# Performance work log

Measured on AMD Instinct MI355X. Metric: run time of the kernel, lower is better.

Reference implementation:

```python
import jax, jax.numpy as jnp
import numpy as np

B, T, F = 256, 288, 64
UNITS = [128, 64, 64, 32]
SCALE = 0.05  # small init so relu-activated recurrence stays numerically stable


def _lstm_scan(x_tbf, Wk, Wr, b):
    """Keras LSTM with activation=relu, recurrent_activation=sigmoid.
    x_tbf: [T, B, in]. Returns all hidden states [T, B, u].
    Gate order in the fused kernel is (i, f, g, o), as in Keras."""
    u = Wr.shape[0]
    bsz = x_tbf.shape[1]

    def step(carry, xt):
        h, c = carry
        z = xt @ Wk + h @ Wr + b            # [B, 4u]
        i, f, g, o = jnp.split(z, 4, axis=-1)
        i = jax.nn.sigmoid(i)
        f = jax.nn.sigmoid(f)
        g = jax.nn.relu(g)                   # cell-input activation = relu
        o = jax.nn.sigmoid(o)
        c = f * c + i * g
        h = o * jax.nn.relu(c)               # output activation = relu
        return (h, c), h

    init = (jnp.zeros((bsz, u), x_tbf.dtype), jnp.zeros((bsz, u), x_tbf.dtype))
    _, hs = jax.lax.scan(step, init, x_tbf)
    return hs  # [T, B, u]


def setup_inputs() -> dict:
    key = jax.random.key(0)
    ks = jax.random.split(key, 20)
    out = {"x": jax.random.normal(ks[0], (B, T, F), dtype=jnp.float32)}
    ins = [F] + UNITS[:-1]
    ki = 1
    for li, (din, u) in enumerate(zip(ins, UNITS), start=1):
        out[f"W{li}"] = jax.random.normal(ks[ki], (din, 4 * u), jnp.float32) * SCALE; ki += 1
        out[f"U{li}"] = jax.random.normal(ks[ki], (u, 4 * u), jnp.float32) * SCALE; ki += 1
        out[f"b{li}"] = jnp.zeros((4 * u,), jnp.float32)
    out["Wf"] = jax.random.normal(ks[ki], (UNITS[-1], 16), jnp.float32) * SCALE; ki += 1
    out["bf"] = jnp.zeros((16,), jnp.float32)
    out["Wo"] = jax.random.normal(ks[ki], (16, 1), jnp.float32) * SCALE
    out["bo"] = jnp.zeros((1,), jnp.float32)
    return out


def reference(x, W1, U1, b1, W2, U2, b2, W3, U3, b3, W4, U4, b4, Wf, bf, Wo, bo):
    # Dropout layers are identity at inference (Keras deterministic call).
    h = jnp.transpose(x, (1, 0, 2))          # [T, B, F] time-major for scan
    h = _lstm_scan(h, W1, U1, b1)            # [T, B, 128]
    h = _lstm_scan(h, W2, U2, b2)            # [T, B, 64]
    h = _lstm_scan(h, W3, U3, b3)            # [T, B, 64]
    h_last = _lstm_scan(h, W4, U4, b4)[-1]   # [B, 32] (return_sequences=False)
    fc = jax.nn.relu(h_last @ Wf + bf)       # [B, 16]
    return fc @ Wo + bo                      # [B, 1]
```

## Files before the change

kernel.cpp:

```cpp
#include <hip/hip_runtime.h>
#include <math.h>

#define TSTEPS 288
#define NTHREADS 512

typedef float f32x2 __attribute__((ext_vector_type(2)));

__device__ __forceinline__ float sigmoidf_(float x) {
    return 1.0f / (1.0f + __expf(-x));
}

__device__ __forceinline__ void pkfma(f32x2& acc, f32x2 w, f32x2 x) {
    asm("v_pk_fma_f32 %0, %1, %2, %0" : "+v"(acc) : "v"(w), "v"(x));
}

template<int NS>
__device__ __forceinline__ float allreduce_seg(float v) {
    if constexpr (NS > 1)
        v += __int_as_float(__builtin_amdgcn_update_dpp(
                0, __float_as_int(v), 0xB1, 0xF, 0xF, true));
    if constexpr (NS > 2)
        v += __int_as_float(__builtin_amdgcn_update_dpp(
                0, __float_as_int(v), 0x4E, 0xF, 0xF, true));
    if constexpr (NS > 4)
        v += __int_as_float(__builtin_amdgcn_ds_swizzle(
                __float_as_int(v), 0x101F));
    return v;
}

template<int NS, int KSEG>
__device__ __forceinline__ int perm_idx(int j) {
    return (((j % KSEG) >> 2) * NS + (j / KSEG)) * 4 + (j & 3);
}

template<int DIN, int U, int NS, int ACTIVE, int SEQNS, int SEQK,
         bool FIRST, bool WRITE_NOW, bool WRITE_DELAY>
__device__ void run_layer(const float* __restrict__ Wk,
                          const float* __restrict__ Wr,
                          const float* __restrict__ bias,
                          const float* __restrict__ xg,
                          float* __restrict__ seq,
                          float* __restrict__ xh,
                          float* __restrict__ xring,
                          int tid)
{
    constexpr int KIN  = DIN / NS;
    constexpr int KH   = U / NS;
    constexpr int COLS = 4 * U;
    constexpr int S    = (NS == 4) ? 2 : 3;
    constexpr int NPI  = KIN / 2;
    constexpr int NPH  = KH / 2;
    static_assert(ACTIVE == NS * U, "thread mapping");
    static_assert(KIN % 4 == 0 && (KH % 4 == 0), "float4 alignment");
    static_assert(NS <= 8, "butterfly width");

    const int seg = tid & (NS - 1);
    const int u   = tid >> S;
    const bool act = tid < ACTIVE;

    f32x2 w[4][NPI + NPH];
    float bz[4] = {0.f, 0.f, 0.f, 0.f};
    float cst = 0.0f, hprev = 0.0f;

    if (act) {
#pragma unroll
        for (int p = 0; p < NPI; ++p) {
            const int k0 = seg * KIN + 2 * p;
#pragma unroll
            for (int g = 0; g < 4; ++g) {
                const int c = g * U + u;
                w[g][p] = f32x2{Wk[(size_t)k0 * COLS + c],
                                Wk[(size_t)(k0 + 1) * COLS + c]};
            }
        }
#pragma unroll
        for (int p = 0; p < NPH; ++p) {
            const int k0 = seg * KH + 2 * p;
#pragma unroll
            for (int g = 0; g < 4; ++g) {
                const int c = g * U + u;
                w[g][NPI + p] = f32x2{Wr[(size_t)k0 * COLS + c],
                                      Wr[(size_t)(k0 + 1) * COLS + c]};
            }
        }
        if (seg == 0) {
#pragma unroll
            for (int g = 0; g < 4; ++g) bz[g] = bias[g * U + u];
        }
#pragma unroll
        for (int g = 0; g < 4; ++g)
#pragma unroll
            for (int p = 0; p < NPI + NPH; ++p)
                asm volatile("" : "+v"(w[g][p]));
    }
    if (tid < 128) xh[tid] = 0.0f;
    if (FIRST && tid < 64)
        xring[perm_idx<4, 16>(tid)] = xg[tid];
    __syncthreads();

    for (int t = 0; t < TSTEPS; ++t) {
        if (act) {
            const float* __restrict__ xr = xh + (t & 1) * 128;
            float* __restrict__ xw       = xh + ((t + 1) & 1) * 128;

            float xstage = 0.0f;
            if (FIRST && tid < 64 && (t + 1) < TSTEPS)
                xstage = xg[(t + 1) * 64 + tid];

            f32x2 ac0 = {0.f, 0.f}, ac1 = {0.f, 0.f},
                  ac2 = {0.f, 0.f}, ac3 = {0.f, 0.f};

            {
                const float4* in4 = reinterpret_cast<const float4*>(
                    FIRST ? (xring + (t & 1) * 64) : (seq + t * 128)) + seg;
#pragma unroll
                for (int k4 = 0; k4 < KIN / 4; ++k4) {
                    const float4 v = in4[k4 * NS];
                    const f32x2 lo = {v.x, v.y}, hi = {v.z, v.w};
                    pkfma(ac0, w[0][2*k4+0], lo); pkfma(ac0, w[0][2*k4+1], hi);
                    pkfma(ac1, w[1][2*k4+0], lo); pkfma(ac1, w[1][2*k4+1], hi);
                    pkfma(ac2, w[2][2*k4+0], lo); pkfma(ac2, w[2][2*k4+1], hi);
                    pkfma(ac3, w[3][2*k4+0], lo); pkfma(ac3, w[3][2*k4+1], hi);
                }
            }
            {
                const float4* h4 = reinterpret_cast<const float4*>(xr) + seg;
#pragma unroll
                for (int k4 = 0; k4 < KH / 4; ++k4) {
                    const float4 v = h4[k4 * NS];
                    const f32x2 lo = {v.x, v.y}, hi = {v.z, v.w};
                    const int pb = NPI + 2 * k4;
                    pkfma(ac0, w[0][pb], lo); pkfma(ac0, w[0][pb+1], hi);
                    pkfma(ac1, w[1][pb], lo); pkfma(ac1, w[1][pb+1], hi);
                    pkfma(ac2, w[2][pb], lo); pkfma(ac2, w[2][pb+1], hi);
                    pkfma(ac3, w[3][pb], lo); pkfma(ac3, w[3][pb+1], hi);
                }
            }

            float a0 = (ac0[0] + ac0[1]) + bz[0];
            float a1 = (ac1[0] + ac1[1]) + bz[1];
            float a2 = (ac2[0] + ac2[1]) + bz[2];
            float a3 = (ac3[0] + ac3[1]) + bz[3];
            a0 = allreduce_seg<NS>(a0);
            a1 = allreduce_seg<NS>(a1);
            a2 = allreduce_seg<NS>(a2);
            a3 = allreduce_seg<NS>(a3);

            if constexpr (WRITE_DELAY) {
                if (seg == 0 && t > 0)
                    seq[(t - 1) * 128 + perm_idx<SEQNS, SEQK>(u)] = hprev;
            }

            const float gi = sigmoidf_(a0);
            const float gf = sigmoidf_(a1);
            const float gg = fmaxf(a2, 0.0f);
            const float go = sigmoidf_(a3);
            cst = fmaf(gf, cst, gi * gg);
            const float h = go * fmaxf(cst, 0.0f);

            if (seg == 0) {
                xw[perm_idx<NS, KH>(u)] = h;
                if constexpr (WRITE_NOW)
                    seq[t * 128 + perm_idx<SEQNS, SEQK>(u)] = h;
            }
            hprev = h;

            if (FIRST && tid < 64 && (t + 1) < TSTEPS)
                xring[((t + 1) & 1) * 64 + perm_idx<4, 16>(tid)] = xstage;
        }
        __syncthreads();
    }

    if constexpr (WRITE_DELAY) {
        if (act && seg == 0)
            seq[(TSTEPS - 1) * 128 + perm_idx<SEQNS, SEQK>(u)] = hprev;
    }
}

extern "C" __global__ void __launch_bounds__(NTHREADS, 2)
lstm_stack_kernel(const float* __restrict__ x,
                  const float* __restrict__ W1, const float* __restrict__ U1, const float* __restrict__ b1,
                  const float* __restrict__ W2, const float* __restrict__ U2, const float* __restrict__ b2,
                  const float* __restrict__ W3, const float* __restrict__ U3, const float* __restrict__ b3,
                  const float* __restrict__ W4, const float* __restrict__ U4, const float* __restrict__ b4,
                  const float* __restrict__ Wf, const float* __restrict__ bf,
                  const float* __restrict__ Wo, const float* __restrict__ bo,
                  float* __restrict__ out)
{
    __shared__ __align__(16) float seq[TSTEPS * 128];
    __shared__ __align__(16) float xh[256 + 16];
    __shared__ __align__(16) float xring[2 * 64];

    const int tid = threadIdx.x;
    const float* xg = x + (size_t)blockIdx.x * TSTEPS * 64;

    run_layer< 64, 128, 4, 512,  8, 16, true , true , false>(W1, U1, b1, xg, seq, xh, xring, tid);
    __syncthreads();
    run_layer<128,  64, 8, 512,  8,  8, false, false, true >(W2, U2, b2, xg, seq, xh, xring, tid);
    __syncthreads();
    run_layer< 64,  64, 8, 512,  8,  8, false, false, true >(W3, U3, b3, xg, seq, xh, xring, tid);
    __syncthreads();
    run_layer< 64,  32, 8, 256,  8,  8, false, false, false>(W4, U4, b4, xg, seq, xh, xring, tid);
    __syncthreads();

    if (tid < 16) {
        float acc = bf[tid];
#pragma unroll
        for (int k = 0; k < 32; ++k) acc = fmaf(xh[k], Wf[k * 16 + tid], acc);
        xh[256 + tid] = fmaxf(acc, 0.0f);
    }
    __syncthreads();
    if (tid == 0) {
        float acc = bo[0];
#pragma unroll
        for (int k = 0; k < 16; ++k) acc = fmaf(xh[256 + k], Wo[k], acc);
        out[blockIdx.x] = acc;
    }
}

extern "C" void kernel_launch(void* const* d_in, const int* in_sizes, int n_in,
                              void* d_out, int out_size, void* d_ws, size_t ws_size,
                              hipStream_t stream) {
    const float* x  = (const float*)d_in[0];
    const float* W1 = (const float*)d_in[1];
    const float* U1 = (const float*)d_in[2];
    const float* b1 = (const float*)d_in[3];
    const float* W2 = (const float*)d_in[4];
    const float* U2 = (const float*)d_in[5];
    const float* b2 = (const float*)d_in[6];
    const float* W3 = (const float*)d_in[7];
    const float* U3 = (const float*)d_in[8];
    const float* b3 = (const float*)d_in[9];
    const float* W4 = (const float*)d_in[10];
    const float* U4 = (const float*)d_in[11];
    const float* b4 = (const float*)d_in[12];
    const float* Wf = (const float*)d_in[13];
    const float* bf = (const float*)d_in[14];
    const float* Wo = (const float*)d_in[15];
    const float* bo = (const float*)d_in[16];
    float* out = (float*)d_out;

    lstm_stack_kernel<<<dim3(256), dim3(NTHREADS), 0, stream>>>(
        x, W1, U1, b1, W2, U2, b2, W3, U3, b3, W4, U4, b4, Wf, bf, Wo, bo, out);
}
```

Measured before the change: 713.5 us.

## Split gate columns across thread pairs and double block size to 1024

Each hidden unit's four gate columns are now split across two thread groups (i,f vs g,o), halving per-thread weights and FMAs and doubling the block to 1024 threads. After the segmented reduction, the pair exchanges gate pre-activations with a ds_swizzle so both halves can compute the cell update, and only one writes h. This shortens the serial per-step critical path of the recurrence, at the cost of an extra cross-lane exchange, a wider __syncthreads barrier each timestep, and launch bounds of 4 waves per SIMD that constrain register use.

```diff
diff --git a/kernel.cpp b/kernel.cpp
--- a/kernel.cpp
+++ b/kernel.cpp
@@ -2,7 +2,7 @@
 #include <math.h>
 
 #define TSTEPS 288
-#define NTHREADS 512
+#define NTHREADS 1024
 
 typedef float f32x2 __attribute__((ext_vector_type(2)));
 
@@ -26,6 +26,12 @@
         v += __int_as_float(__builtin_amdgcn_ds_swizzle(
                 __float_as_int(v), 0x101F));
     return v;
+}
+
+template<int NS>
+__device__ __forceinline__ float swz_pair(float v) {
+    return __int_as_float(__builtin_amdgcn_ds_swizzle(
+        __float_as_int(v), (NS << 10) | 0x1F));
 }
 
 template<int NS, int KSEG>
@@ -47,51 +53,49 @@
     constexpr int KIN  = DIN / NS;
     constexpr int KH   = U / NS;
     constexpr int COLS = 4 * U;
-    constexpr int S    = (NS == 4) ? 2 : 3;
+    constexpr int LOG  = (NS == 4) ? 2 : 3;
     constexpr int NPI  = KIN / 2;
     constexpr int NPH  = KH / 2;
-    static_assert(ACTIVE == NS * U, "thread mapping");
-    static_assert(KIN % 4 == 0 && (KH % 4 == 0), "float4 alignment");
-    static_assert(NS <= 8, "butterfly width");
+    constexpr int NP   = NPI + NPH;
+    static_assert(ACTIVE == 2 * U * NS, "thread mapping");
+    static_assert(KIN % 4 == 0 && KH % 4 == 0, "float4 alignment");
+    static_assert(NS == 4 || NS == 8, "butterfly width");
 
     const int seg = tid & (NS - 1);
-    const int u   = tid >> S;
+    const int p   = (tid >> LOG) & 1;
+    const int u   = tid >> (LOG + 1);
     const bool act = tid < ACTIVE;
 
-    f32x2 w[4][NPI + NPH];
-    float bz[4] = {0.f, 0.f, 0.f, 0.f};
+    f32x2 w[2][NP];
+    float bz[2] = {0.f, 0.f};
     float cst = 0.0f, hprev = 0.0f;
 
     if (act) {
-#pragma unroll
-        for (int p = 0; p < NPI; ++p) {
-            const int k0 = seg * KIN + 2 * p;
-#pragma unroll
-            for (int g = 0; g < 4; ++g) {
-                const int c = g * U + u;
-                w[g][p] = f32x2{Wk[(size_t)k0 * COLS + c],
-                                Wk[(size_t)(k0 + 1) * COLS + c]};
-            }
+        const int colA = (2 * p) * U + u;
+        const int colB = (2 * p + 1) * U + u;
+#pragma unroll
+        for (int q = 0; q < NPI; ++q) {
+            const int k0 = seg * KIN + 2 * q;
+            w[0][q] = f32x2{Wk[(size_t)k0 * COLS + colA],
+                            Wk[(size_t)(k0 + 1) * COLS + colA]};
+            w[1][q] = f32x2{Wk[(size_t)k0 * COLS + colB],
+                            Wk[(size_t)(k0 + 1) * COLS + colB]};
         }
 #pragma unroll
-        for (int p = 0; p < NPH; ++p) {
-            const int k0 = seg * KH + 2 * p;
-#pragma unroll
-            for (int g = 0; g < 4; ++g) {
-                const int c = g * U + u;
-                w[g][NPI + p] = f32x2{Wr[(size_t)k0 * COLS + c],
-                                      Wr[(size_t)(k0 + 1) * COLS + c]};
-            }
+        for (int q = 0; q < NPH; ++q) {
+            const int k0 = seg * KH + 2 * q;
+            w[0][NPI + q] = f32x2{Wr[(size_t)k0 * COLS + colA],
+                                  Wr[(size_t)(k0 + 1) * COLS + colA]};
+            w[1][NPI + q] = f32x2{Wr[(size_t)k0 * COLS + colB],
+                                  Wr[(size_t)(k0 + 1) * COLS + colB]};
         }
-        if (seg == 0) {
-#pragma unroll
-            for (int g = 0; g < 4; ++g) bz[g] = bias[g * U + u];
-        }
-#pragma unroll
-        for (int g = 0; g < 4; ++g)
-#pragma unroll
-            for (int p = 0; p < NPI + NPH; ++p)
-                asm volatile("" : "+v"(w[g][p]));
+        bz[0] = bias[colA];
+        bz[1] = bias[colB];
+#pragma unroll
+        for (int g = 0; g < 2; ++g)
+#pragma unroll
+            for (int q = 0; q < NP; ++q)
+                asm volatile("" : "+v"(w[g][q]));
     }
     if (tid < 128) xh[tid] = 0.0f;
     if (FIRST && tid < 64)
@@ -107,8 +111,7 @@
             if (FIRST && tid < 64 && (t + 1) < TSTEPS)
                 xstage = xg[(t + 1) * 64 + tid];
 
-            f32x2 ac0 = {0.f, 0.f}, ac1 = {0.f, 0.f},
-                  ac2 = {0.f, 0.f}, ac3 = {0.f, 0.f};
+            f32x2 ac0 = {0.f, 0.f}, ac1 = {0.f, 0.f};
 
             {
                 const float4* in4 = reinterpret_cast<const float4*>(
@@ -119,8 +122,6 @@
                     const f32x2 lo = {v.x, v.y}, hi = {v.z, v.w};
                     pkfma(ac0, w[0][2*k4+0], lo); pkfma(ac0, w[0][2*k4+1], hi);
                     pkfma(ac1, w[1][2*k4+0], lo); pkfma(ac1, w[1][2*k4+1], hi);
-                    pkfma(ac2, w[2][2*k4+0], lo); pkfma(ac2, w[2][2*k4+1], hi);
-                    pkfma(ac3, w[3][2*k4+0], lo); pkfma(ac3, w[3][2*k4+1], hi);
                 }
             }
             {
@@ -132,33 +133,34 @@
                     const int pb = NPI + 2 * k4;
                     pkfma(ac0, w[0][pb], lo); pkfma(ac0, w[0][pb+1], hi);
                     pkfma(ac1, w[1][pb], lo); pkfma(ac1, w[1][pb+1], hi);
-                    pkfma(ac2, w[2][pb], lo); pkfma(ac2, w[2][pb+1], hi);
-                    pkfma(ac3, w[3][pb], lo); pkfma(ac3, w[3][pb+1], hi);
                 }
             }
 
-            float a0 = (ac0[0] + ac0[1]) + bz[0];
-            float a1 = (ac1[0] + ac1[1]) + bz[1];
-            float a2 = (ac2[0] + ac2[1]) + bz[2];
-            float a3 = (ac3[0] + ac3[1]) + bz[3];
-            a0 = allreduce_seg<NS>(a0);
-            a1 = allreduce_seg<NS>(a1);
-            a2 = allreduce_seg<NS>(a2);
-            a3 = allreduce_seg<NS>(a3);
+            float a0 = (ac0[0] + ac0[1]);
+            float a1 = (ac1[0] + ac1[1]);
+            a0 = allreduce_seg<NS>(a0) + bz[0];
+            a1 = allreduce_seg<NS>(a1) + bz[1];
+
+            const float r0 = swz_pair<NS>(a0);
+            const float r1 = swz_pair<NS>(a1);
+            const float zi = p ? r0 : a0;
+            const float zf = p ? r1 : a1;
+            const float zg = p ? a0 : r0;
+            const float zo = p ? a1 : r1;
 
             if constexpr (WRITE_DELAY) {
-                if (seg == 0 && t > 0)
+                if (seg == 0 && p == 0 && t > 0)
                     seq[(t - 1) * 128 + perm_idx<SEQNS, SEQK>(u)] = hprev;
             }
 
-            const float gi = sigmoidf_(a0);
-            const float gf = sigmoidf_(a1);
-            const float gg = fmaxf(a2, 0.0f);
-            const float go = sigmoidf_(a3);
+            const float gi = sigmoidf_(zi);
+            const float gf = sigmoidf_(zf);
+            const float gg = fmaxf(zg, 0.0f);
+            const float go = sigmoidf_(zo);
             cst = fmaf(gf, cst, gi * gg);
             const float h = go * fmaxf(cst, 0.0f);
 
-            if (seg == 0) {
+            if (seg == 0 && p == 0) {
                 xw[perm_idx<NS, KH>(u)] = h;
                 if constexpr (WRITE_NOW)
                     seq[t * 128 + perm_idx<SEQNS, SEQK>(u)] = h;
@@ -172,12 +174,12 @@
     }
 
     if constexpr (WRITE_DELAY) {
-        if (act && seg == 0)
+        if (act && seg == 0 && p == 0)
             seq[(TSTEPS - 1) * 128 + perm_idx<SEQNS, SEQK>(u)] = hprev;
     }
 }
 
-extern "C" __global__ void __launch_bounds__(NTHREADS, 2)
+extern "C" __global__ void __launch_bounds__(NTHREADS, 4)
 lstm_stack_kernel(const float* __restrict__ x,
                   const float* __restrict__ W1, const float* __restrict__ U1, const float* __restrict__ b1,
                   const float* __restrict__ W2, const float* __restrict__ U2, const float* __restrict__ b2,
@@ -194,13 +196,13 @@
     const int tid = threadIdx.x;
     const float* xg = x + (size_t)blockIdx.x * TSTEPS * 64;
 
-    run_layer< 64, 128, 4, 512,  8, 16, true , true , false>(W1, U1, b1, xg, seq, xh, xring, tid);
-    __syncthreads();
-    run_layer<128,  64, 8, 512,  8,  8, false, false, true >(W2, U2, b2, xg, seq, xh, xring, tid);
-    __syncthreads();
-    run_layer< 64,  64, 8, 512,  8,  8, false, false, true >(W3, U3, b3, xg, seq, xh, xring, tid);
-    __syncthreads();
-    run_layer< 64,  32, 8, 256,  8,  8, false, false, false>(W4, U4, b4, xg, seq, xh, xring, tid);
+    run_layer< 64, 128, 4, 1024, 8, 16, true , true , false>(W1, U1, b1, xg, seq, xh, xring, tid);
+    __syncthreads();
+    run_layer<128,  64, 8, 1024, 8,  8, false, false, true >(W2, U2, b2, xg, seq, xh, xring, tid);
+    __syncthreads();
+    run_layer< 64,  64, 8, 1024, 8,  8, false, false, true >(W3, U3, b3, xg, seq, xh, xring, tid);
+    __syncthreads();
+    run_layer< 64,  32, 8,  512, 8,  8, false, false, false>(W4, U4, b4, xg, seq, xh, xring, tid);
     __syncthreads();
 
     if (tid < 16) {
```

After: 967.1 us. 1.36x slower.

## Pipeline LSTM layers 2-4 as a wavefront across split thread groups

Applied to the files above, without the earlier changes.

Layer 1 still runs over the whole sequence with all 512 threads. Layers 2, 3 and 4 then run at the same time: threads 0-255 compute layer 2 while threads 256-511 compute layers 3 and 4, each lagging one timestep behind the layer feeding it, with one block barrier per step. This replaces three sequential 288-step passes with a single 290-step pipelined pass, cutting barriers and serial latency. In exchange each thread holds more weights in registers, and layer 2 uses a coarser split (4 segments instead of 8), which lengthens each step.

```diff
diff --git a/kernel.cpp b/kernel.cpp
--- a/kernel.cpp
+++ b/kernel.cpp
@@ -33,123 +33,169 @@
     return (((j % KSEG) >> 2) * NS + (j / KSEG)) * 4 + (j & 3);
 }
 
-template<int DIN, int U, int NS, int ACTIVE, int SEQNS, int SEQK,
-         bool FIRST, bool WRITE_NOW, bool WRITE_DELAY>
-__device__ void run_layer(const float* __restrict__ Wk,
-                          const float* __restrict__ Wr,
-                          const float* __restrict__ bias,
-                          const float* __restrict__ xg,
-                          float* __restrict__ seq,
-                          float* __restrict__ xh,
-                          float* __restrict__ xring,
-                          int tid)
+__device__ void run_l1(const float* __restrict__ Wk, const float* __restrict__ Wr,
+                       const float* __restrict__ bias, const float* __restrict__ xg,
+                       float* __restrict__ seq, float* __restrict__ xh,
+                       float* __restrict__ xring, int tid)
 {
-    constexpr int KIN  = DIN / NS;
-    constexpr int KH   = U / NS;
-    constexpr int COLS = 4 * U;
-    constexpr int S    = (NS == 4) ? 2 : 3;
-    constexpr int NPI  = KIN / 2;
-    constexpr int NPH  = KH / 2;
-    static_assert(ACTIVE == NS * U, "thread mapping");
-    static_assert(KIN % 4 == 0 && (KH % 4 == 0), "float4 alignment");
-    static_assert(NS <= 8, "butterfly width");
-
-    const int seg = tid & (NS - 1);
-    const int u   = tid >> S;
-    const bool act = tid < ACTIVE;
-
-    f32x2 w[4][NPI + NPH];
-    float bz[4] = {0.f, 0.f, 0.f, 0.f};
-    float cst = 0.0f, hprev = 0.0f;
-
-    if (act) {
-#pragma unroll
-        for (int p = 0; p < NPI; ++p) {
-            const int k0 = seg * KIN + 2 * p;
-#pragma unroll
-            for (int g = 0; g < 4; ++g) {
-                const int c = g * U + u;
-                w[g][p] = f32x2{Wk[(size_t)k0 * COLS + c],
-                                Wk[(size_t)(k0 + 1) * COLS + c]};
-            }
-        }
-#pragma unroll
-        for (int p = 0; p < NPH; ++p) {
-            const int k0 = seg * KH + 2 * p;
-#pragma unroll
-            for (int g = 0; g < 4; ++g) {
-                const int c = g * U + u;
-                w[g][NPI + p] = f32x2{Wr[(size_t)k0 * COLS + c],
-                                      Wr[(size_t)(k0 + 1) * COLS + c]};
-            }
-        }
+    constexpr int U = 128, COLS = 512, NPI = 8, NPH = 16, NP = NPI + NPH;
+    const int seg = tid & 3;
+    const int u   = tid >> 2;
+
+    f32x2 w[4][NP];
+#pragma unroll
+    for (int q = 0; q < NPI; ++q) {
+        const int k0 = seg * 16 + 2 * q;
+#pragma unroll
+        for (int g = 0; g < 4; ++g)
+            w[g][q] = f32x2{Wk[(size_t)k0 * COLS + g * U + u],
+                            Wk[(size_t)(k0 + 1) * COLS + g * U + u]};
+    }
+#pragma unroll
+    for (int q = 0; q < NPH; ++q) {
+        const int k0 = seg * 32 + 2 * q;
+#pragma unroll
+        for (int g = 0; g < 4; ++g)
+            w[g][NPI + q] = f32x2{Wr[(size_t)k0 * COLS + g * U + u],
+                                  Wr[(size_t)(k0 + 1) * COLS + g * U + u]};
+    }
+    float bz[4];
+#pragma unroll
+    for (int g = 0; g < 4; ++g) bz[g] = bias[g * U + u];
+#pragma unroll
+    for (int g = 0; g < 4; ++g)
+#pragma unroll
+        for (int q = 0; q < NP; ++q)
+            asm volatile("" : "+v"(w[g][q]));
+
+    float cst = 0.0f;
+
+    for (int t = 0; t < TSTEPS; ++t) {
+        const float* __restrict__ xr = xh + (t & 1) * 128;
+        float* __restrict__ xw       = xh + ((t + 1) & 1) * 128;
+
+        float xstage = 0.0f;
+        if (tid < 64 && (t + 1) < TSTEPS) xstage = xg[(t + 1) * 64 + tid];
+
+        f32x2 ac0 = {0.f,0.f}, ac1 = {0.f,0.f}, ac2 = {0.f,0.f}, ac3 = {0.f,0.f};
+
+        {
+            const float4* in4 = reinterpret_cast<const float4*>(xring + (t & 1) * 64) + seg;
+#pragma unroll
+            for (int k = 0; k < 4; ++k) {
+                const float4 v = in4[k * 4];
+                const f32x2 lo = {v.x, v.y}, hi = {v.z, v.w};
+                pkfma(ac0, w[0][2*k],   lo); pkfma(ac0, w[0][2*k+1], hi);
+                pkfma(ac1, w[1][2*k],   lo); pkfma(ac1, w[1][2*k+1], hi);
+                pkfma(ac2, w[2][2*k],   lo); pkfma(ac2, w[2][2*k+1], hi);
+                pkfma(ac3, w[3][2*k],   lo); pkfma(ac3, w[3][2*k+1], hi);
+            }
+        }
+        {
+            const float4* h4 = reinterpret_cast<const float4*>(xr) + seg;
+#pragma unroll
+            for (int k = 0; k < 8; ++k) {
+                const float4 v = h4[k * 4];
+                const f32x2 lo = {v.x, v.y}, hi = {v.z, v.w};
+                const int pb = NPI + 2 * k;
+                pkfma(ac0, w[0][pb], lo); pkfma(ac0, w[0][pb+1], hi);
+                pkfma(ac1, w[1][pb], lo); pkfma(ac1, w[1][pb+1], hi);
+                pkfma(ac2, w[2][pb], lo); pkfma(ac2, w[2][pb+1], hi);
+                pkfma(ac3, w[3][pb], lo); pkfma(ac3, w[3][pb+1], hi);
+            }
+        }
+        float a0 = allreduce_seg<4>(ac0[0] + ac0[1]) + bz[0];
+        float a1 = allreduce_seg<4>(ac1[0] + ac1[1]) + bz[1];
+        float a2 = allreduce_seg<4>(ac2[0] + ac2[1]) + bz[2];
+        float a3 = allreduce_seg<4>(ac3[0] + ac3[1]) + bz[3];
+
+        const float gi = sigmoidf_(a0);
+        const float gf = sigmoidf_(a1);
+        const float gg = fmaxf(a2, 0.0f);
+        const float go = sigmoidf_(a3);
+        cst = fmaf(gf, cst, gi * gg);
+        const float h = go * fmaxf(cst, 0.0f);
+
         if (seg == 0) {
-#pragma unroll
-            for (int g = 0; g < 4; ++g) bz[g] = bias[g * U + u];
-        }
-#pragma unroll
-        for (int g = 0; g < 4; ++g)
-#pragma unroll
-            for (int p = 0; p < NPI + NPH; ++p)
-                asm volatile("" : "+v"(w[g][p]));
-    }
-    if (tid < 128) xh[tid] = 0.0f;
-    if (FIRST && tid < 64)
-        xring[perm_idx<4, 16>(tid)] = xg[tid];
-    __syncthreads();
-
-    for (int t = 0; t < TSTEPS; ++t) {
-        if (act) {
-            const float* __restrict__ xr = xh + (t & 1) * 128;
-            float* __restrict__ xw       = xh + ((t + 1) & 1) * 128;
-
-            float xstage = 0.0f;
-            if (FIRST && tid < 64 && (t + 1) < TSTEPS)
-                xstage = xg[(t + 1) * 64 + tid];
-
-            f32x2 ac0 = {0.f, 0.f}, ac1 = {0.f, 0.f},
-                  ac2 = {0.f, 0.f}, ac3 = {0.f, 0.f};
-
-            {
-                const float4* in4 = reinterpret_cast<const float4*>(
-                    FIRST ? (xring + (t & 1) * 64) : (seq + t * 128)) + seg;
-#pragma unroll
-                for (int k4 = 0; k4 < KIN / 4; ++k4) {
-                    const float4 v = in4[k4 * NS];
+            const int pj = perm_idx<4, 32>(u);
+            xw[pj] = h;
+            seq[t * 128 + pj] = h;
+        }
+        if (tid < 64 && (t + 1) < TSTEPS)
+            xring[((t + 1) & 1) * 64 + perm_idx<4, 16>(tid)] = xstage;
+        __syncthreads();
+    }
+}
+
+__device__ void fused_l2(const float* __restrict__ Wk, const float* __restrict__ Wr,
+                         const float* __restrict__ bias,
+                         const float* __restrict__ seq, float* __restrict__ xh2,
+                         int lt)
+{
+    constexpr int U = 64, COLS = 256, NPI = 16, NPH = 8, NP = NPI + NPH;
+    const int seg = lt & 3;
+    const int u   = lt >> 2;
+
+    f32x2 w[4][NP];
+#pragma unroll
+    for (int q = 0; q < NPI; ++q) {
+        const int k0 = seg * 32 + 2 * q;
+#pragma unroll
+        for (int g = 0; g < 4; ++g)
+            w[g][q] = f32x2{Wk[(size_t)k0 * COLS + g * U + u],
+                            Wk[(size_t)(k0 + 1) * COLS + g * U + u]};
+    }
+#pragma unroll
+    for (int q = 0; q < NPH; ++q) {
+        const int k0 = seg * 16 + 2 * q;
+#pragma unroll
+        for (int g = 0; g < 4; ++g)
+            w[g][NPI + q] = f32x2{Wr[(size_t)k0 * COLS + g * U + u],
+                                  Wr[(size_t)(k0 + 1) * COLS + g * U + u]};
+    }
+    float bz[4];
+#pragma unroll
+    for (int g = 0; g < 4; ++g) bz[g] = bias[g * U + u];
+#pragma unroll
+    for (int g = 0; g < 4; ++g)
+#pragma unroll
+        for (int q = 0; q < NP; ++q)
+            asm volatile("" : "+v"(w[g][q]));
+
+    float cst = 0.0f;
+
+    for (int i = 0; i < TSTEPS + 2; ++i) {
+        if (i < TSTEPS) {
+            f32x2 ac0 = {0.f,0.f}, ac1 = {0.f,0.f}, ac2 = {0.f,0.f}, ac3 = {0.f,0.f};
+            {
+                const float4* in4 = reinterpret_cast<const float4*>(seq + i * 128) + seg;
+#pragma unroll
+                for (int k = 0; k < 8; ++k) {
+                    const float4 v = in4[k * 4];
                     const f32x2 lo = {v.x, v.y}, hi = {v.z, v.w};
-                    pkfma(ac0, w[0][2*k4+0], lo); pkfma(ac0, w[0][2*k4+1], hi);
-                    pkfma(ac1, w[1][2*k4+0], lo); pkfma(ac1, w[1][2*k4+1], hi);
-                    pkfma(ac2, w[2][2*k4+0], lo); pkfma(ac2, w[2][2*k4+1], hi);
-                    pkfma(ac3, w[3][2*k4+0], lo); pkfma(ac3, w[3][2*k4+1], hi);
+                    pkfma(ac0, w[0][2*k],   lo); pkfma(ac0, w[0][2*k+1], hi);
+                    pkfma(ac1, w[1][2*k],   lo); pkfma(ac1, w[1][2*k+1], hi);
+                    pkfma(ac2, w[2][2*k],   lo); pkfma(ac2, w[2][2*k+1], hi);
+                    pkfma(ac3, w[3][2*k],   lo); pkfma(ac3, w[3][2*k+1], hi);
                 }
             }
             {
-                const float4* h4 = reinterpret_cast<const float4*>(xr) + seg;
-#pragma unroll
-                for (int k4 = 0; k4 < KH / 4; ++k4) {
-                    const float4 v = h4[k4 * NS];
+                const float4* h4 = reinterpret_cast<const float4*>(xh2 + ((i + 1) & 1) * 64) + seg;
+#pragma unroll
+                for (int k = 0; k < 4; ++k) {
+                    const float4 v = h4[k * 4];
                     const f32x2 lo = {v.x, v.y}, hi = {v.z, v.w};
-                    const int pb = NPI + 2 * k4;
+                    const int pb = NPI + 2 * k;
                     pkfma(ac0, w[0][pb], lo); pkfma(ac0, w[0][pb+1], hi);
                     pkfma(ac1, w[1][pb], lo); pkfma(ac1, w[1][pb+1], hi);
                     pkfma(ac2, w[2][pb], lo); pkfma(ac2, w[2][pb+1], hi);
                     pkfma(ac3, w[3][pb], lo); pkfma(ac3, w[3][pb+1], hi);
                 }
             }
-
-            float a0 = (ac0[0] + ac0[1]) + bz[0];
-            float a1 = (ac1[0] + ac1[1]) + bz[1];
-            float a2 = (ac2[0] + ac2[1]) + bz[2];
-            float a3 = (ac3[0] + ac3[1]) + bz[3];
-            a0 = allreduce_seg<NS>(a0);
-            a1 = allreduce_seg<NS>(a1);
-            a2 = allreduce_seg<NS>(a2);
-            a3 = allreduce_seg<NS>(a3);
-
-            if constexpr (WRITE_DELAY) {
-                if (seg == 0 && t > 0)
-                    seq[(t - 1) * 128 + perm_idx<SEQNS, SEQK>(u)] = hprev;
-            }
+            float a0 = allreduce_seg<4>(ac0[0] + ac0[1]) + bz[0];
+            float a1 = allreduce_seg<4>(ac1[0] + ac1[1]) + bz[1];
+            float a2 = allreduce_seg<4>(ac2[0] + ac2[1]) + bz[2];
+            float a3 = allreduce_seg<4>(ac3[0] + ac3[1]) + bz[3];
 
             const float gi = sigmoidf_(a0);
             const float gf = sigmoidf_(a1);
@@ -158,22 +204,144 @@
             cst = fmaf(gf, cst, gi * gg);
             const float h = go * fmaxf(cst, 0.0f);
 
-            if (seg == 0) {
-                xw[perm_idx<NS, KH>(u)] = h;
-                if constexpr (WRITE_NOW)
-                    seq[t * 128 + perm_idx<SEQNS, SEQK>(u)] = h;
-            }
-            hprev = h;
-
-            if (FIRST && tid < 64 && (t + 1) < TSTEPS)
-                xring[((t + 1) & 1) * 64 + perm_idx<4, 16>(tid)] = xstage;
+            if (seg == 0) xh2[(i & 1) * 64 + perm_idx<4, 16>(u)] = h;
         }
         __syncthreads();
     }
-
-    if constexpr (WRITE_DELAY) {
-        if (act && seg == 0)
-            seq[(TSTEPS - 1) * 128 + perm_idx<SEQNS, SEQK>(u)] = hprev;
+}
+
+__device__ void fused_l34(const float* __restrict__ W3k, const float* __restrict__ W3r,
+                          const float* __restrict__ b3,
+                          const float* __restrict__ W4k, const float* __restrict__ W4r,
+                          const float* __restrict__ b4,
+                          const float* __restrict__ xh2, float* __restrict__ xh3,
+                          float* __restrict__ xh4, int lt)
+{
+    const int seg3 = lt & 3,  u3 = lt >> 2;
+    const int seg4 = lt & 7,  u4 = lt >> 3;
+
+    f32x2 w3[4][16];
+#pragma unroll
+    for (int q = 0; q < 8; ++q) {
+        const int k0 = seg3 * 16 + 2 * q;
+#pragma unroll
+        for (int g = 0; g < 4; ++g)
+            w3[g][q] = f32x2{W3k[(size_t)k0 * 256 + g * 64 + u3],
+                             W3k[(size_t)(k0 + 1) * 256 + g * 64 + u3]};
+    }
+#pragma unroll
+    for (int q = 0; q < 8; ++q) {
+        const int k0 = seg3 * 16 + 2 * q;
+#pragma unroll
+        for (int g = 0; g < 4; ++g)
+            w3[g][8 + q] = f32x2{W3r[(size_t)k0 * 256 + g * 64 + u3],
+                                 W3r[(size_t)(k0 + 1) * 256 + g * 64 + u3]};
+    }
+    f32x2 w4[4][6];
+#pragma unroll
+    for (int q = 0; q < 4; ++q) {
+        const int k0 = seg4 * 8 + 2 * q;
+#pragma unroll
+        for (int g = 0; g < 4; ++g)
+            w4[g][q] = f32x2{W4k[(size_t)k0 * 128 + g * 32 + u4],
+                             W4k[(size_t)(k0 + 1) * 128 + g * 32 + u4]};
+    }
+#pragma unroll
+    for (int q = 0; q < 2; ++q) {
+        const int k0 = seg4 * 4 + 2 * q;
+#pragma unroll
+        for (int g = 0; g < 4; ++g)
+            w4[g][4 + q] = f32x2{W4r[(size_t)k0 * 128 + g * 32 + u4],
+                                 W4r[(size_t)(k0 + 1) * 128 + g * 32 + u4]};
+    }
+    float bz3[4], bz4[4];
+#pragma unroll
+    for (int g = 0; g < 4; ++g) { bz3[g] = b3[g * 64 + u3]; bz4[g] = b4[g * 32 + u4]; }
+#pragma unroll
+    for (int g = 0; g < 4; ++g) {
+#pragma unroll
+        for (int q = 0; q < 16; ++q) asm volatile("" : "+v"(w3[g][q]));
+#pragma unroll
+        for (int q = 0; q < 6;  ++q) asm volatile("" : "+v"(w4[g][q]));
+    }
+
+    float c3 = 0.0f, c4 = 0.0f;
+
+    for (int i = 0; i < TSTEPS + 2; ++i) {
+        if (i >= 1 && i <= TSTEPS) {
+            f32x2 ac0 = {0.f,0.f}, ac1 = {0.f,0.f}, ac2 = {0.f,0.f}, ac3 = {0.f,0.f};
+            {
+                const float4* in4 = reinterpret_cast<const float4*>(xh2 + ((i - 1) & 1) * 64) + seg3;
+#pragma unroll
+                for (int k = 0; k < 4; ++k) {
+                    const float4 v = in4[k * 4];
+                    const f32x2 lo = {v.x, v.y}, hi = {v.z, v.w};
+                    pkfma(ac0, w3[0][2*k],   lo); pkfma(ac0, w3[0][2*k+1], hi);
+                    pkfma(ac1, w3[1][2*k],   lo); pkfma(ac1, w3[1][2*k+1], hi);
+                    pkfma(ac2, w3[2][2*k],   lo); pkfma(ac2, w3[2][2*k+1], hi);
+                    pkfma(ac3, w3[3][2*k],   lo); pkfma(ac3, w3[3][2*k+1], hi);
+                }
+            }
+            {
+                const float4* h4 = reinterpret_cast<const float4*>(xh3 + (i & 1) * 64) + seg3;
+#pragma unroll
+                for (int k = 0; k < 4; ++k) {
+                    const float4 v = h4[k * 4];
+                    const f32x2 lo = {v.x, v.y}, hi = {v.z, v.w};
+                    const int pb = 8 + 2 * k;
+                    pkfma(ac0, w3[0][pb], lo); pkfma(ac0, w3[0][pb+1], hi);
+                    pkfma(ac1, w3[1][pb], lo); pkfma(ac1, w3[1][pb+1], hi);
+                    pkfma(ac2, w3[2][pb], lo); pkfma(ac2, w3[2][pb+1], hi);
+                    pkfma(ac3, w3[3][pb], lo); pkfma(ac3, w3[3][pb+1], hi);
+                }
+            }
+            float a0 = allreduce_seg<4>(ac0[0] + ac0[1]) + bz3[0];
+            float a1 = allreduce_seg<4>(ac1[0] + ac1[1]) + bz3[1];
+            float a2 = allreduce_seg<4>(ac2[0] + ac2[1]) + bz3[2];
+            float a3 = allreduce_seg<4>(ac3[0] + ac3[1]) + bz3[3];
+            const float gi = sigmoidf_(a0);
+            const float gf = sigmoidf_(a1);
+            const float gg = fmaxf(a2, 0.0f);
+            const float go = sigmoidf_(a3);
+            c3 = fmaf(gf, c3, gi * gg);
+            const float h = go * fmaxf(c3, 0.0f);
+            if (seg3 == 0) xh3[((i - 1) & 1) * 64 + perm_idx<4, 16>(u3)] = h;
+        }
+        if (i >= 2) {
+            f32x2 ac0 = {0.f,0.f}, ac1 = {0.f,0.f}, ac2 = {0.f,0.f}, ac3 = {0.f,0.f};
+            {
+                const float4* in4 = reinterpret_cast<const float4*>(xh3 + (i & 1) * 64);
+#pragma unroll
+                for (int k = 0; k < 2; ++k) {
+                    const float4 v = in4[((seg4 & 1) * 2 + k) * 4 + (seg4 >> 1)];
+                    const f32x2 lo = {v.x, v.y}, hi = {v.z, v.w};
+                    pkfma(ac0, w4[0][2*k],   lo); pkfma(ac0, w4[0][2*k+1], hi);
+                    pkfma(ac1, w4[1][2*k],   lo); pkfma(ac1, w4[1][2*k+1], hi);
+                    pkfma(ac2, w4[2][2*k],   lo); pkfma(ac2, w4[2][2*k+1], hi);
+                    pkfma(ac3, w4[3][2*k],   lo); pkfma(ac3, w4[3][2*k+1], hi);
+                }
+            }
+            {
+                const float4 v = reinterpret_cast<const float4*>(xh4 + ((i - 1) & 1) * 32)[seg4];
+                const f32x2 lo = {v.x, v.y}, hi = {v.z, v.w};
+                pkfma(ac0, w4[0][4], lo); pkfma(ac0, w4[0][5], hi);
+                pkfma(ac1, w4[1][4], lo); pkfma(ac1, w4[1][5], hi);
+                pkfma(ac2, w4[2][4], lo); pkfma(ac2, w4[2][5], hi);
+                pkfma(ac3, w4[3][4], lo); pkfma(ac3, w4[3][5], hi);
+            }
+            float a0 = allreduce_seg<8>(ac0[0] + ac0[1]) + bz4[0];
+            float a1 = allreduce_seg<8>(ac1[0] + ac1[1]) + bz4[1];
+            float a2 = allreduce_seg<8>(ac2[0] + ac2[1]) + bz4[2];
+            float a3 = allreduce_seg<8>(ac3[0] + ac3[1]) + bz4[3];
+            const float gi = sigmoidf_(a0);
+            const float gf = sigmoidf_(a1);
+            const float gg = fmaxf(a2, 0.0f);
+            const float go = sigmoidf_(a3);
+            c4 = fmaf(gf, c4, gi * gg);
+            const float h = go * fmaxf(c4, 0.0f);
+            if (seg4 == 0) xh4[(i & 1) * 32 + u4] = h;
+        }
+        __syncthreads();
     }
 }
 
@@ -188,32 +356,42 @@
                   float* __restrict__ out)
 {
     __shared__ __align__(16) float seq[TSTEPS * 128];
-    __shared__ __align__(16) float xh[256 + 16];
+    __shared__ __align__(16) float xh1[2 * 128];
     __shared__ __align__(16) float xring[2 * 64];
+    __shared__ __align__(16) float xh2[2 * 64];
+    __shared__ __align__(16) float xh3[2 * 64];
+    __shared__ __align__(16) float xh4[2 * 32];
+    __shared__ __align__(16) float hbuf[16];
 
     const int tid = threadIdx.x;
     const float* xg = x + (size_t)blockIdx.x * TSTEPS * 64;
 
-    run_layer< 64, 128, 4, 512,  8, 16, true , true , false>(W1, U1, b1, xg, seq, xh, xring, tid);
+    if (tid < 128) xh1[tid] = 0.0f;
+    if (tid < 64) {
+        xring[perm_idx<4, 16>(tid)] = xg[tid];
+        xh2[64 + tid] = 0.0f;
+        xh3[64 + tid] = 0.0f;
+    }
+    if (tid < 32) xh4[32 + tid] = 0.0f;
     __syncthreads();
-    run_layer<128,  64, 8, 512,  8,  8, false, false, true >(W2, U2, b2, xg, seq, xh, xring, tid);
-    __syncthreads();
-    run_layer< 64,  64, 8, 512,  8,  8, false, false, true >(W3, U3, b3, xg, seq, xh, xring, tid);
-    __syncthreads();
-    run_layer< 64,  32, 8, 256,  8,  8, false, false, false>(W4, U4, b4, xg, seq, xh, xring, tid);
+
+    run_l1(W1, U1, b1, xg, seq, xh1, xring, tid);
+
+    if (tid < 256) fused_l2(W2, U2, b2, seq, xh2, tid);
+    else           fused_l34(W3, U3, b3, W4, U4, b4, xh2, xh3, xh4, tid - 256);
     __syncthreads();
 
     if (tid < 16) {
         float acc = bf[tid];
 #pragma unroll
-        for (int k = 0; k < 32; ++k) acc = fmaf(xh[k], Wf[k * 16 + tid], acc);
-        xh[256 + tid] = fmaxf(acc, 0.0f);
+        for (int k = 0; k < 32; ++k) acc = fmaf(xh4[32 + k], Wf[k * 16 + tid], acc);
+        hbuf[tid] = fmaxf(acc, 0.0f);
     }
     __syncthreads();
     if (tid == 0) {
         float acc = bo[0];
 #pragma unroll
-        for (int k = 0; k < 16; ++k) acc = fmaf(xh[256 + k], Wo[k], acc);
+        for (int k = 0; k < 16; ++k) acc = fmaf(hbuf[k], Wo[k], acc);
         out[blockIdx.x] = acc;
     }
 }
```

Result: faster. 576.2 us (-19.3%).
